# Optimization experiments

Measured on AMD Instinct MI355X. Metric: run time of the kernel, lower is better.

Reference implementation:

```python
import jax, jax.numpy as jnp
import numpy as np

WS = 8
NH = 6

def _ln(x, g, b, eps=1e-5):
    m = x.mean(-1, keepdims=True)
    v = jnp.var(x, axis=-1, keepdims=True)
    return (x - m) / jnp.sqrt(v + eps) * g + b

def _dwconv(x_nchw, k):
    # depthwise 3x3, stride 1, padding 1 (SAME); k: (C,1,3,3)
    return jax.lax.conv_general_dilated(
        x_nchw, k, (1, 1), 'SAME',
        dimension_numbers=('NCHW', 'OIHW', 'NCHW'),
        feature_group_count=x_nchw.shape[1])

def setup_inputs() -> dict:
    key = jax.random.key(0)
    ks = jax.random.split(key, 12)
    B, H, W, C = 2, 256, 256, 180
    hd_ffn = 360
    s = 0.02
    return {
        'x': jax.random.normal(ks[0], (B, H * W, C), jnp.float32),
        'w_qkv': jax.random.normal(ks[1], (3 * C, C), jnp.float32) * s,
        'b_rel': jax.random.normal(ks[2], (NH, WS * WS, WS * WS), jnp.float32) * s,
        'w_proj': jax.random.normal(ks[3], (C, C), jnp.float32) * s,
        'b_proj': jnp.zeros((C,), jnp.float32),
        'conv_dw': jax.random.normal(ks[4], (C, 1, 3, 3), jnp.float32) * 0.1,
        'cg_w1': jax.random.normal(ks[5], (C // 8, C), jnp.float32) * s,
        'cg_w2': jax.random.normal(ks[6], (C, C // 8), jnp.float32) * s,
        'ffn_w1': jax.random.normal(ks[7], (hd_ffn, C), jnp.float32) * s,
        'ffn_dw': jax.random.normal(ks[8], (hd_ffn, 1, 3, 3), jnp.float32) * 0.1,
        'ffn_w2': jax.random.normal(ks[9], (C, hd_ffn), jnp.float32) * s,
        'n1_g': jnp.ones((C,), jnp.float32),
        'n1_b': jnp.zeros((C,), jnp.float32),
        'n2_g': jnp.ones((C,), jnp.float32),
        'n2_b': jnp.zeros((C,), jnp.float32),
        'H': H,
        'W': W,
    }

def reference(x, w_qkv, b_rel, w_proj, b_proj, conv_dw, cg_w1, cg_w2,
              ffn_w1, ffn_dw, ffn_w2, n1_g, n1_b, n2_g, n2_b, H, W):
    B, L, C = x.shape
    hd = C // NH
    scale = hd ** -0.5
    n1 = _ln(x, n1_g, n1_b)
    # --- spatial window attention branch ---
    xw = n1.reshape(B, H // WS, WS, W // WS, WS, C)
    xw = xw.transpose(0, 1, 3, 2, 4, 5).reshape(-1, WS * WS, C)  # (nw, 64, C)
    qkv = (xw @ w_qkv.T).reshape(-1, WS * WS, 3, NH, hd).transpose(2, 0, 3, 1, 4)
    q, k, v = qkv[0], qkv[1], qkv[2]  # (nw, nh, 64, hd)
    attn = jax.nn.softmax((q * scale) @ jnp.swapaxes(k, -2, -1) + b_rel, axis=-1)
    out = (attn @ v).transpose(0, 2, 1, 3).reshape(-1, WS * WS, C)
    out = out @ w_proj.T + b_proj
    attn_feat = out.reshape(B, H // WS, W // WS, WS, WS, C)
    attn_feat = attn_feat.transpose(0, 1, 3, 2, 4, 5).reshape(B, L, C)
    # --- conv branch: depthwise 3x3 + GELU ---
    nchw = n1.transpose(0, 2, 1).reshape(B, C, H, W)
    conv_feat = jax.nn.gelu(_dwconv(nchw, conv_dw), approximate=False)
    conv_feat = conv_feat.reshape(B, C, L).transpose(0, 2, 1)
    # --- AIM: channel gate on conv_feat modulates attn_feat ---
    pooled = conv_feat.mean(axis=1)  # (B, C) == AdaptiveAvgPool2d(1)
    cm = jax.nn.sigmoid(jax.nn.gelu(pooled @ cg_w1.T, approximate=False) @ cg_w2.T)
    x = x + (attn_feat * cm[:, None, :] + conv_feat)
    # --- FFN with depthwise spatial mixing ---
    n2 = _ln(x, n2_g, n2_b)
    h = jax.nn.gelu(n2 @ ffn_w1.T, approximate=False)  # (B, L, hd_ffn)
    hdim = h.shape[-1]
    h_s = _dwconv(h.transpose(0, 2, 1).reshape(B, hdim, H, W), ffn_dw)
    h_s = h_s.reshape(B, hdim, L).transpose(0, 2, 1)
    return x + h_s @ ffn_w2.T
```

## Files before the change

kernel.cpp:

```cpp
#include <hip/hip_runtime.h>
#include <hip/hip_bf16.h>
#include <math.h>

#define BATCH 2
#define IMG 256
#define LTOK 65536
#define CH 180
#define BL (BATCH * LTOK)
#define HDF 360

using frag_ab = __attribute__((ext_vector_type(8))) short;
using frag_cd = __attribute__((ext_vector_type(4))) float;

__device__ __forceinline__ float b2f(unsigned short u) {
    union { unsigned int i; float f; } v; v.i = ((unsigned int)u) << 16; return v.f;
}
__device__ __forceinline__ float blo(unsigned int u) {
    union { unsigned int i; float f; } v; v.i = u << 16; return v.f;
}
__device__ __forceinline__ float bhi(unsigned int u) {
    union { unsigned int i; float f; } v; v.i = u & 0xffff0000u; return v.f;
}
__device__ __forceinline__ unsigned short f2b(float f) {
    union { float f; unsigned int i; } v; v.f = f;
    unsigned int x = v.i;
    unsigned int r = (x + 0x7fffu + ((x >> 16) & 1u)) >> 16;
    return (unsigned short)r;
}
__device__ __forceinline__ float gelu_f(float x) {
    return 0.5f * x * (1.0f + erff(x * 0.70710678118654752f));
}

template <int PERM>
__device__ __forceinline__ int perm_row(int row) {
    if (PERM == 1) {
        int b = row >> 16, l = row & 65535;
        int y = l >> 8, x = l & 255;
        return (b << 16) + ((((y >> 3) << 5) + (x >> 3)) << 6) + ((y & 7) << 3) + (x & 7);
    } else if (PERM == 2) {
        int b = row >> 16, wv = row & 65535;
        int wid = wv >> 6, t = wv & 63;
        int wy = wid >> 5, wx = wid & 31;
        return (b << 16) + ((((wy << 3) + (t >> 3))) << 8) + (wx << 3) + (t & 7);
    }
    return row;
}

__global__ __launch_bounds__(256) void convw_kernel(
    const float* __restrict__ a, const float* __restrict__ b,
    const float* __restrict__ c, const float* __restrict__ d,
    const float* __restrict__ cdw, const float* __restrict__ fdw,
    const float* __restrict__ brel,
    unsigned short* __restrict__ wbf, float* __restrict__ wT1, float* __restrict__ wT2,
    unsigned short* __restrict__ br3)
{
    int g = blockIdx.x * 256 + threadIdx.x;
    if (g < 259200) {
        float v;
        if      (g < 97200)  v = a[g];
        else if (g < 129600) v = b[g - 97200];
        else if (g < 194400) v = c[g - 129600];
        else                 v = d[g - 194400];
        wbf[g] = f2b(v);
    } else if (g < 265680) {
        int i = g - 259200;
        int tap = i / 180, ch = i % 180;
        wT1[i] = cdw[ch * 9 + tap];
    } else if (g < 278640) {
        int i = g - 265680;
        int tap = i / 360, ch = i % 360;
        wT2[i] = fdw[ch * 9 + tap];
    } else if (g < 303216) {
        int i = g - 278640;
        int h = i >> 12;
        int rem = i & 4095;
        int lane = rem >> 6;
        int j = rem & 63;
        int mt = j >> 4, nt = (j >> 2) & 3, r = j & 3;
        int row = mt * 16 + (lane >> 4) * 4 + r;
        int col = nt * 16 + (lane & 15);
        br3[i] = f2b(brel[h * 4096 + row * 64 + col]);
    }
}

__device__ __forceinline__ void ld4(const float* p, float v[4]) {
    float4 t = *(const float4*)p; v[0]=t.x; v[1]=t.y; v[2]=t.z; v[3]=t.w;
}
__device__ __forceinline__ void ld4(const unsigned short* p, float v[4]) {
    ushort4 t = *(const ushort4*)p; v[0]=b2f(t.x); v[1]=b2f(t.y); v[2]=b2f(t.z); v[3]=b2f(t.w);
}

template <typename TIN>
__global__ __launch_bounds__(256) void ln_kernel(
    const TIN* __restrict__ x, const float* __restrict__ g,
    const float* __restrict__ bta, unsigned short* __restrict__ out)
{
    int wave = threadIdx.x >> 6, lane = threadIdx.x & 63;
    int tok = blockIdx.x * 4 + wave;
    const bool act = lane < 45;
    float v[4] = {0.f, 0.f, 0.f, 0.f};
    const TIN* row = x + (size_t)tok * CH;
    if (act) ld4(row + lane * 4, v);
    float s  = v[0] + v[1] + v[2] + v[3];
    float sq = v[0]*v[0] + v[1]*v[1] + v[2]*v[2] + v[3]*v[3];
    #pragma unroll
    for (int off = 32; off > 0; off >>= 1) {
        s  += __shfl_xor(s, off);
        sq += __shfl_xor(sq, off);
    }
    float mean = s * (1.f / CH);
    float var  = sq * (1.f / CH) - mean * mean;
    float rstd = rsqrtf(var + 1e-5f);
    if (act) {
        float4 gg = *(const float4*)&g[lane * 4];
        float4 bb = *(const float4*)&bta[lane * 4];
        unsigned int o0 = (unsigned int)f2b((v[0]-mean)*rstd*gg.x + bb.x)
                        | ((unsigned int)f2b((v[1]-mean)*rstd*gg.y + bb.y) << 16);
        unsigned int o1 = (unsigned int)f2b((v[2]-mean)*rstd*gg.z + bb.z)
                        | ((unsigned int)f2b((v[3]-mean)*rstd*gg.w + bb.w) << 16);
        *(uint2*)(out + (size_t)tok * CH + lane * 4) = make_uint2(o0, o1);
    }
}

__device__ __forceinline__ void stv(float* p, float v) { *p = v; }
__device__ __forceinline__ void stv(unsigned short* p, float v) { *p = f2b(v); }

__device__ __forceinline__ frag_ab ldg_frag(const unsigned short* p) {
    union { frag_ab f; uint2 u[2]; } t;
    t.u[0] = *(const uint2*)p;
    t.u[1] = *(const uint2*)(p + 4);
    return t.f;
}
__device__ __forceinline__ frag_ab ldg_frag_tail(const unsigned short* p, int kcol0, int K) {
    union { frag_ab f; unsigned short s[8]; } t;
    #pragma unroll
    for (int j = 0; j < 8; ++j)
        t.s[j] = (kcol0 + j < K) ? p[j] : (unsigned short)0;
    return t.f;
}

template <int KT, int ACT, bool HAS_BIAS, bool HAS_RES, int PERM, typename TOUT>
__global__ __launch_bounds__(256) void gemm_kernel(
    const unsigned short* __restrict__ X, int ldx,
    const unsigned short* __restrict__ Wt,
    const float* __restrict__ bias,
    const unsigned short* __restrict__ res, int ldr,
    TOUT* __restrict__ Y, int ldy,
    int N)
{
    constexpr int NCH  = KT / 32;
    constexpr bool TAIL = (KT % 32) != 0;
    constexpr int NFR  = NCH + (TAIL ? 1 : 0);

    const int tid = threadIdx.x;
    const int wave = tid >> 6;
    const int lane = tid & 63;
    const int l16 = lane & 15;
    const int q = lane >> 4;
    const int m0 = blockIdx.x * 128;
    const int ktail0 = NCH * 32 + q * 8;

    frag_ab areg[2][NFR];
    {
        const unsigned short* aptr0 = X + (size_t)(m0 + wave * 32 + l16) * ldx + q * 8;
        const unsigned short* aptr1 = aptr0 + (size_t)16 * ldx;
        #pragma unroll
        for (int kc = 0; kc < NCH; ++kc) {
            areg[0][kc] = ldg_frag(aptr0 + kc * 32);
            areg[1][kc] = ldg_frag(aptr1 + kc * 32);
        }
        if (TAIL) {
            areg[0][NFR - 1] = ldg_frag_tail(aptr0 + NCH * 32, ktail0, KT);
            areg[1][NFR - 1] = ldg_frag_tail(aptr1 + NCH * 32, ktail0, KT);
        }
    }

    for (int n0 = 0; n0 < N; n0 += 64) {
        frag_cd acc[2][4];
        #pragma unroll
        for (int mb = 0; mb < 2; ++mb)
            #pragma unroll
            for (int nb = 0; nb < 4; ++nb)
                acc[mb][nb] = (frag_cd){0.f, 0.f, 0.f, 0.f};

        const unsigned short* bptr[4];
        #pragma unroll
        for (int nb = 0; nb < 4; ++nb)
            bptr[nb] = Wt + (size_t)(n0 + nb * 16 + l16) * KT + q * 8;

        #pragma unroll
        for (int kc = 0; kc < NCH; ++kc) {
            #pragma unroll
            for (int nb = 0; nb < 4; ++nb) {
                frag_ab b = ldg_frag(bptr[nb] + kc * 32);
                acc[0][nb] = __builtin_amdgcn_mfma_f32_16x16x32_bf16(areg[0][kc], b, acc[0][nb], 0, 0, 0);
                acc[1][nb] = __builtin_amdgcn_mfma_f32_16x16x32_bf16(areg[1][kc], b, acc[1][nb], 0, 0, 0);
            }
        }
        if (TAIL) {
            #pragma unroll
            for (int nb = 0; nb < 4; ++nb) {
                frag_ab b = ldg_frag_tail(bptr[nb] + NCH * 32, ktail0, KT);
                acc[0][nb] = __builtin_amdgcn_mfma_f32_16x16x32_bf16(areg[0][NFR - 1], b, acc[0][nb], 0, 0, 0);
                acc[1][nb] = __builtin_amdgcn_mfma_f32_16x16x32_bf16(areg[1][NFR - 1], b, acc[1][nb], 0, 0, 0);
            }
        }

        #pragma unroll
        for (int nb = 0; nb < 4; ++nb) {
            const int col = n0 + nb * 16 + l16;
            if (col < N) {
                float bv = 0.f;
                if (HAS_BIAS) bv = bias[col];
                #pragma unroll
                for (int mb = 0; mb < 2; ++mb) {
                    #pragma unroll
                    for (int r = 0; r < 4; ++r) {
                        int row = m0 + wave * 32 + mb * 16 + q * 4 + r;
                        int orow = perm_row<PERM>(row);
                        float v = acc[mb][nb][r] + bv;
                        if (ACT == 1) v = gelu_f(v);
                        if (HAS_RES) v += b2f(res[(size_t)orow * ldr + col]);
                        stv(&Y[(size_t)orow * ldy + col], v);
                    }
                }
            }
        }
    }
}

__global__ __launch_bounds__(64) void attn_kernel(
    const unsigned short* __restrict__ qkvw,
    const unsigned short* __restrict__ br3,
    unsigned short* __restrict__ attn_out)
{
    __shared__ unsigned short Pl[64][72];
    __shared__ unsigned short VT[32][72];
    const int blk = blockIdx.x;
    const int h = blk % 6;
    const int w = blk / 6;
    const int lane = threadIdx.x;
    const int l16 = lane & 15;
    const int g4 = lane >> 4;
    const float scale = 0.18257418583505536f;

    const unsigned short* base = qkvw + (size_t)w * (64 * 540) + h * 30;

    frag_ab qf[4], kf[4];
    #pragma unroll
    for (int t = 0; t < 4; ++t) {
        const unsigned short* pq = base + (size_t)(t * 16 + l16) * 540 + g4 * 8;
        union { frag_ab f; uint2 u[2]; } tq, tk;
        tq.u[0] = *(const uint2*)pq;        tq.u[1] = *(const uint2*)(pq + 4);
        tk.u[0] = *(const uint2*)(pq + 180); tk.u[1] = *(const uint2*)(pq + 184);
        if (g4 == 3) { tk.f[6] = 0; tk.f[7] = 0; }
        qf[t] = tq.f; kf[t] = tk.f;
    }

    unsigned int brw[32];
    {
        const unsigned short* bp = br3 + ((size_t)h << 12) + lane * 64;
        #pragma unroll
        for (int c2 = 0; c2 < 8; ++c2)
            *(uint4*)&brw[c2 * 4] = *(const uint4*)(bp + c2 * 8);
    }

    frag_cd s[4][4];
    #pragma unroll
    for (int mt = 0; mt < 4; ++mt)
        #pragma unroll
        for (int nt = 0; nt < 4; ++nt)
            s[mt][nt] = (frag_cd){0.f, 0.f, 0.f, 0.f};
    #pragma unroll
    for (int mt = 0; mt < 4; ++mt)
        #pragma unroll
        for (int nt = 0; nt < 4; ++nt)
            s[mt][nt] = __builtin_amdgcn_mfma_f32_16x16x32_bf16(qf[mt], kf[nt], s[mt][nt], 0, 0, 0);

    {
        const unsigned short* pv = base + (size_t)lane * 540 + 360;
        #pragma unroll
        for (int d2 = 0; d2 < 15; ++d2) {
            unsigned int u = *(const unsigned int*)(pv + 2 * d2);
            VT[2 * d2][lane]     = (unsigned short)(u & 0xffffu);
            VT[2 * d2 + 1][lane] = (unsigned short)(u >> 16);
        }
        VT[30][lane] = 0; VT[31][lane] = 0;
    }

    float inv[4][4];
    #pragma unroll
    for (int mt = 0; mt < 4; ++mt) {
        #pragma unroll
        for (int r = 0; r < 4; ++r) {
            float a0 = s[mt][0][r] * scale + (((0 * 4 + r) & 1) ? bhi(brw[(mt * 16 + 0 + r) >> 1]) : blo(brw[(mt * 16 + 0 + r) >> 1]));
            float a1 = s[mt][1][r] * scale + (((1 * 4 + r) & 1) ? bhi(brw[(mt * 16 + 4 + r) >> 1]) : blo(brw[(mt * 16 + 4 + r) >> 1]));
            float a2 = s[mt][2][r] * scale + (((2 * 4 + r) & 1) ? bhi(brw[(mt * 16 + 8 + r) >> 1]) : blo(brw[(mt * 16 + 8 + r) >> 1]));
            float a3 = s[mt][3][r] * scale + (((3 * 4 + r) & 1) ? bhi(brw[(mt * 16 + 12 + r) >> 1]) : blo(brw[(mt * 16 + 12 + r) >> 1]));
            float m = fmaxf(fmaxf(a0, a1), fmaxf(a2, a3));
            m = fmaxf(m, __shfl_xor(m, 1));
            m = fmaxf(m, __shfl_xor(m, 2));
            m = fmaxf(m, __shfl_xor(m, 4));
            m = fmaxf(m, __shfl_xor(m, 8));
            float e0 = __expf(a0 - m), e1 = __expf(a1 - m);
            float e2 = __expf(a2 - m), e3 = __expf(a3 - m);
            float sum = e0 + e1 + e2 + e3;
            sum += __shfl_xor(sum, 1);
            sum += __shfl_xor(sum, 2);
            sum += __shfl_xor(sum, 4);
            sum += __shfl_xor(sum, 8);
            inv[mt][r] = 1.f / sum;
            int row = mt * 16 + g4 * 4 + r;
            Pl[row][l16]      = f2b(e0);
            Pl[row][16 + l16] = f2b(e1);
            Pl[row][32 + l16] = f2b(e2);
            Pl[row][48 + l16] = f2b(e3);
        }
    }
    __syncthreads();

    frag_ab pf[4][2];
    #pragma unroll
    for (int mt = 0; mt < 4; ++mt)
        #pragma unroll
        for (int kt = 0; kt < 2; ++kt)
            pf[mt][kt] = *(const frag_ab*)&Pl[mt * 16 + l16][kt * 32 + g4 * 8];
    frag_ab vf[2][2];
    #pragma unroll
    for (int nt = 0; nt < 2; ++nt)
        #pragma unroll
        for (int kt = 0; kt < 2; ++kt)
            vf[nt][kt] = *(const frag_ab*)&VT[nt * 16 + l16][kt * 32 + g4 * 8];

    frag_cd o[4][2];
    #pragma unroll
    for (int mt = 0; mt < 4; ++mt)
        #pragma unroll
        for (int nt = 0; nt < 2; ++nt)
            o[mt][nt] = (frag_cd){0.f, 0.f, 0.f, 0.f};
    #pragma unroll
    for (int mt = 0; mt < 4; ++mt)
        #pragma unroll
        for (int nt = 0; nt < 2; ++nt)
            #pragma unroll
            for (int kt = 0; kt < 2; ++kt)
                o[mt][nt] = __builtin_amdgcn_mfma_f32_16x16x32_bf16(pf[mt][kt], vf[nt][kt], o[mt][nt], 0, 0, 0);

    unsigned short* ob = attn_out + (size_t)w * (64 * CH) + h * 30;
    #pragma unroll
    for (int mt = 0; mt < 4; ++mt) {
        #pragma unroll
        for (int r = 0; r < 4; ++r) {
            int row = mt * 16 + g4 * 4 + r;
            float iv = inv[mt][r];
            unsigned short* op = ob + (size_t)row * CH;
            op[l16] = f2b(o[mt][0][r] * iv);
            if (l16 < 14) op[16 + l16] = f2b(o[mt][1][r] * iv);
        }
    }
}

template <int C, bool DO_GELU>
__global__ __launch_bounds__(256) void dwconv_kernel(
    const unsigned short* __restrict__ in, const float* __restrict__ wT,
    unsigned short* __restrict__ out)
{
    constexpr int NG = (C + 7) / 8;
    constexpr int TY = 8;
    int gid = blockIdx.x * 256 + threadIdx.x;
    int cg = gid % NG;
    int t  = gid / NG;
    int x  = t % IMG;
    int t2 = t / IMG;
    int yb = t2 & 31;
    int bi = t2 >> 5;
    if (bi >= BATCH) return;
    const int c0 = cg * 8;
    const int y0 = yb * TY;

    float w9[9][8];
    #pragma unroll
    for (int tp = 0; tp < 9; ++tp) {
        float4 wa = *(const float4*)&wT[tp * C + c0];
        float4 wb = *(const float4*)&wT[tp * C + c0 + 4];
        w9[tp][0]=wa.x; w9[tp][1]=wa.y; w9[tp][2]=wa.z; w9[tp][3]=wa.w;
        w9[tp][4]=wb.x; w9[tp][5]=wb.y; w9[tp][6]=wb.z; w9[tp][7]=wb.w;
    }

    unsigned int rr[3][3][4];

    auto load_row = [&](int y, unsigned int dst[3][4]) {
        if ((unsigned)y >= (unsigned)IMG) {
            #pragma unroll
            for (int cc = 0; cc < 3; ++cc)
                #pragma unroll
                for (int k = 0; k < 4; ++k) dst[cc][k] = 0u;
            return;
        }
        size_t base = ((size_t)((bi << 16) + (y << 8) + x)) * C + c0;
        #pragma unroll
        for (int cc = 0; cc < 3; ++cc) {
            int xx = x + cc - 1;
            if ((unsigned)xx >= (unsigned)IMG) {
                dst[cc][0] = dst[cc][1] = dst[cc][2] = dst[cc][3] = 0u;
                continue;
            }
            const unsigned short* p = in + base + (ptrdiff_t)(cc - 1) * C;
            uint2 u0 = *(const uint2*)p;
            uint2 u1 = *(const uint2*)(p + 4);
            dst[cc][0] = u0.x; dst[cc][1] = u0.y; dst[cc][2] = u1.x; dst[cc][3] = u1.y;
        }
    };

    load_row(y0 - 1, rr[0]);
    load_row(y0,     rr[1]);

    #pragma unroll
    for (int dy = 0; dy < TY; ++dy) {
        load_row(y0 + dy + 1, rr[(dy + 2) % 3]);
        float acc[8];
        #pragma unroll
        for (int j = 0; j < 8; ++j) acc[j] = 0.f;
        #pragma unroll
        for (int ky = 0; ky < 3; ++ky) {
            unsigned int (*row)[4] = rr[(dy + ky) % 3];
            #pragma unroll
            for (int kx = 0; kx < 3; ++kx) {
                const float* wp = w9[ky * 3 + kx];
                const unsigned int* u = row[kx];
                acc[0] += blo(u[0]) * wp[0];
                acc[1] += bhi(u[0]) * wp[1];
                acc[2] += blo(u[1]) * wp[2];
                acc[3] += bhi(u[1]) * wp[3];
                acc[4] += blo(u[2]) * wp[4];
                acc[5] += bhi(u[2]) * wp[5];
                acc[6] += blo(u[3]) * wp[6];
                acc[7] += bhi(u[3]) * wp[7];
            }
        }
        if (DO_GELU) {
            #pragma unroll
            for (int j = 0; j < 8; ++j) acc[j] = gelu_f(acc[j]);
        }
        size_t ob = ((size_t)((bi << 16) + ((y0 + dy) << 8) + x)) * C + c0;
        unsigned int o0 = (unsigned int)f2b(acc[0]) | ((unsigned int)f2b(acc[1]) << 16);
        unsigned int o1 = (unsigned int)f2b(acc[2]) | ((unsigned int)f2b(acc[3]) << 16);
        *(uint2*)(out + ob) = make_uint2(o0, o1);
        if (c0 + 8 <= C) {
            unsigned int o2 = (unsigned int)f2b(acc[4]) | ((unsigned int)f2b(acc[5]) << 16);
            unsigned int o3 = (unsigned int)f2b(acc[6]) | ((unsigned int)f2b(acc[7]) << 16);
            *(uint2*)(out + ob + 4) = make_uint2(o2, o3);
        }
    }
}

__global__ __launch_bounds__(64) void pool_kernel(
    const unsigned short* __restrict__ cf, float* __restrict__ pooled)
{
    int t = threadIdx.x;
    if (t >= 45) return;
    int b = blockIdx.x >> 7;
    int chunk = blockIdx.x & 127;
    const unsigned short* base = cf + (size_t)(b * LTOK + chunk * 512) * CH + t * 4;
    float s0 = 0.f, s1 = 0.f, s2 = 0.f, s3 = 0.f;
    for (int i = 0; i < 512; ++i) {
        ushort4 v = *(const ushort4*)(base + (size_t)i * CH);
        s0 += b2f(v.x); s1 += b2f(v.y); s2 += b2f(v.z); s3 += b2f(v.w);
    }
    atomicAdd(&pooled[b * CH + t * 4 + 0], s0);
    atomicAdd(&pooled[b * CH + t * 4 + 1], s1);
    atomicAdd(&pooled[b * CH + t * 4 + 2], s2);
    atomicAdd(&pooled[b * CH + t * 4 + 3], s3);
}

__global__ __launch_bounds__(256) void cm_kernel(
    const float* __restrict__ pooled, const float* __restrict__ w1,
    const float* __restrict__ w2, float* __restrict__ cm)
{
    __shared__ float p[BATCH][CH];
    __shared__ float g1[BATCH][22];
    int t = threadIdx.x;
    for (int idx = t; idx < BATCH * CH; idx += 256)
        p[idx / CH][idx % CH] = pooled[idx] * (1.f / (float)LTOK);
    __syncthreads();
    if (t < BATCH * 22) {
        int b = t / 22, u = t % 22;
        float s = 0.f;
        for (int c = 0; c < CH; ++c) s += p[b][c] * w1[u * CH + c];
        g1[b][u] = gelu_f(s);
    }
    __syncthreads();
    for (int idx = t; idx < BATCH * CH; idx += 256) {
        int b = idx / CH, c = idx % CH;
        float s = 0.f;
        for (int u = 0; u < 22; ++u) s += g1[b][u] * w2[c * 22 + u];
        cm[idx] = 1.f / (1.f + __expf(-s));
    }
}

__global__ __launch_bounds__(256) void resid_kernel(
    const float* __restrict__ x, const unsigned short* __restrict__ attn_feat,
    const unsigned short* __restrict__ conv_feat, const float* __restrict__ cm,
    unsigned short* __restrict__ x_mid)
{
    int gid = blockIdx.x * 256 + threadIdx.x;
    int c4 = gid % 45;
    int b = gid / (LTOK * 45);
    float4 xv = ((const float4*)x)[gid];
    ushort4 a = ((const ushort4*)attn_feat)[gid];
    ushort4 c = ((const ushort4*)conv_feat)[gid];
    float4 m = *(const float4*)&cm[b * CH + c4 * 4];
    unsigned int o0 = (unsigned int)f2b(xv.x + b2f(a.x) * m.x + b2f(c.x))
                    | ((unsigned int)f2b(xv.y + b2f(a.y) * m.y + b2f(c.y)) << 16);
    unsigned int o1 = (unsigned int)f2b(xv.z + b2f(a.z) * m.z + b2f(c.z))
                    | ((unsigned int)f2b(xv.w + b2f(a.w) * m.w + b2f(c.w)) << 16);
    ((uint2*)x_mid)[gid] = make_uint2(o0, o1);
}

extern "C" void kernel_launch(void* const* d_in, const int* in_sizes, int n_in,
                              void* d_out, int out_size, void* d_ws, size_t ws_size,
                              hipStream_t stream)
{
    const float* x       = (const float*)d_in[0];
    const float* w_qkv   = (const float*)d_in[1];
    const float* b_rel   = (const float*)d_in[2];
    const float* w_proj  = (const float*)d_in[3];
    const float* b_proj  = (const float*)d_in[4];
    const float* conv_dw = (const float*)d_in[5];
    const float* cg_w1   = (const float*)d_in[6];
    const float* cg_w2   = (const float*)d_in[7];
    const float* ffn_w1  = (const float*)d_in[8];
    const float* ffn_dw  = (const float*)d_in[9];
    const float* ffn_w2  = (const float*)d_in[10];
    const float* n1_g    = (const float*)d_in[11];
    const float* n1_b    = (const float*)d_in[12];
    const float* n2_g    = (const float*)d_in[13];
    const float* n2_b    = (const float*)d_in[14];

    char* ws = (char*)d_ws;
    unsigned short* n1        = (unsigned short*)(ws);
    unsigned short* qkvw      = (unsigned short*)(ws + 47185920);
    unsigned short* conv_feat = (unsigned short*)(ws + 188743680);
    unsigned short* attn_out  = (unsigned short*)(ws);
    unsigned short* attn_feat = (unsigned short*)(ws + 47185920);
    unsigned short* x_mid     = (unsigned short*)(ws + 94371840);
    unsigned short* n2        = (unsigned short*)(ws + 141557760);
    unsigned short* h         = (unsigned short*)(ws);
    unsigned short* h_s       = (unsigned short*)(ws + 141557760);
    float*          pooled    = (float*)(ws + 235929600);
    float*          cmv       = (float*)(ws + 235931040);
    unsigned short* wbf       = (unsigned short*)(ws + 235932480);
    float*          wT1       = (float*)(ws + 236450880);
    float*          wT2       = (float*)(ws + 236476800);
    unsigned short* br3       = (unsigned short*)(ws + 236528640);
    unsigned short* wqkv_b  = wbf;
    unsigned short* wproj_b = wbf + 97200;
    unsigned short* wffn1_b = wbf + 129600;
    unsigned short* wffn2_b = wbf + 194400;
    float* out = (float*)d_out;

    hipMemsetAsync(pooled, 0, 2880, stream);

    convw_kernel<<<1185, 256, 0, stream>>>(w_qkv, w_proj, ffn_w1, ffn_w2,
                                           conv_dw, ffn_dw, b_rel, wbf, wT1, wT2, br3);
    ln_kernel<float><<<BL / 4, 256, 0, stream>>>(x, n1_g, n1_b, n1);
    gemm_kernel<180, 0, false, false, 1, unsigned short><<<BL / 128, 256, 0, stream>>>(
        n1, CH, wqkv_b, nullptr, nullptr, 0, qkvw, 540, 540);
    dwconv_kernel<CH, true><<<1472, 256, 0, stream>>>(n1, wT1, conv_feat);
    pool_kernel<<<BATCH * 128, 64, 0, stream>>>(conv_feat, pooled);
    cm_kernel<<<1, 256, 0, stream>>>(pooled, cg_w1, cg_w2, cmv);
    attn_kernel<<<2048 * 6, 64, 0, stream>>>(qkvw, br3, attn_out);
    gemm_kernel<180, 0, true, false, 2, unsigned short><<<BL / 128, 256, 0, stream>>>(
        attn_out, CH, wproj_b, b_proj, nullptr, 0, attn_feat, CH, CH);
    resid_kernel<<<(BL * CH / 4) / 256, 256, 0, stream>>>(x, attn_feat, conv_feat, cmv, x_mid);
    ln_kernel<unsigned short><<<BL / 4, 256, 0, stream>>>(x_mid, n2_g, n2_b, n2);
    gemm_kernel<180, 1, false, false, 0, unsigned short><<<BL / 128, 256, 0, stream>>>(
        n2, CH, wffn1_b, nullptr, nullptr, 0, h, HDF, HDF);
    dwconv_kernel<HDF, false><<<2880, 256, 0, stream>>>(h, wT2, h_s);
    gemm_kernel<360, 0, false, true, 0, float><<<BL / 128, 256, 0, stream>>>(
        h_s, HDF, wffn2_b, nullptr, x_mid, CH, out, CH, CH);
}
```

Baseline: 951.2 us.

## Fuse QKV projection into window attention and fuse residual with LayerNorm2

Replaces the separate QKV GEMM and per-head attention kernel with one kernel per 8x8 window. It loads the window's n1 rows into registers, computes Q/K/V per head with MFMA into LDS, then runs softmax attention, so the large bf16 qkv intermediate is never written to or read from global memory. The residual-add kernel and the second LayerNorm are also merged into one pass, saving a reread of x_mid. The cost is that each block re-reads the whole QKV weight matrix from global/L2 and serialises the six heads with three barriers per head. The workspace buffers are rearranged to fit.

```diff
diff --git a/kernel.cpp b/kernel.cpp
--- a/kernel.cpp
+++ b/kernel.cpp
@@ -52,7 +52,7 @@
     const float* __restrict__ cdw, const float* __restrict__ fdw,
     const float* __restrict__ brel,
     unsigned short* __restrict__ wbf, float* __restrict__ wT1, float* __restrict__ wT2,
-    unsigned short* __restrict__ br3)
+    unsigned short* __restrict__ br4)
 {
     int g = blockIdx.x * 256 + threadIdx.x;
     if (g < 259200) {
@@ -74,20 +74,18 @@
         int i = g - 278640;
         int h = i >> 12;
         int rem = i & 4095;
-        int lane = rem >> 6;
-        int j = rem & 63;
-        int mt = j >> 4, nt = (j >> 2) & 3, r = j & 3;
-        int row = mt * 16 + (lane >> 4) * 4 + r;
-        int col = nt * 16 + (lane & 15);
-        br3[i] = f2b(brel[h * 4096 + row * 64 + col]);
+        int tid = rem >> 4;
+        int j = rem & 15;
+        int nt = j >> 2, r = j & 3;
+        int w = tid >> 6, q = (tid >> 4) & 3, l16 = tid & 15;
+        int row = w * 16 + q * 4 + r;
+        int col = nt * 16 + l16;
+        br4[i] = f2b(brel[h * 4096 + row * 64 + col]);
     }
 }
 
 __device__ __forceinline__ void ld4(const float* p, float v[4]) {
     float4 t = *(const float4*)p; v[0]=t.x; v[1]=t.y; v[2]=t.z; v[3]=t.w;
-}
-__device__ __forceinline__ void ld4(const unsigned short* p, float v[4]) {
-    ushort4 t = *(const ushort4*)p; v[0]=b2f(t.x); v[1]=b2f(t.y); v[2]=b2f(t.z); v[3]=b2f(t.w);
 }
 
 template <typename TIN>
@@ -229,74 +227,100 @@
     }
 }
 
-__global__ __launch_bounds__(64) void attn_kernel(
-    const unsigned short* __restrict__ qkvw,
-    const unsigned short* __restrict__ br3,
+__global__ __launch_bounds__(256) void qkvattn_kernel(
+    const unsigned short* __restrict__ n1,
+    const unsigned short* __restrict__ wqkv,
+    const unsigned short* __restrict__ br4,
     unsigned short* __restrict__ attn_out)
 {
-    __shared__ unsigned short Pl[64][72];
+    __shared__ unsigned short Klds[64][40];
     __shared__ unsigned short VT[32][72];
+    __shared__ unsigned short Qlds[4][16][40];
+    __shared__ unsigned short Pl[4][16][72];
+
     const int blk = blockIdx.x;
-    const int h = blk % 6;
-    const int w = blk / 6;
-    const int lane = threadIdx.x;
+    const int b = blk >> 10;
+    const int wid = blk & 1023;
+    const int wy = wid >> 5, wx = wid & 31;
+    const int tid = threadIdx.x;
+    const int wave = tid >> 6;
+    const int lane = tid & 63;
     const int l16 = lane & 15;
-    const int g4 = lane >> 4;
+    const int q = lane >> 4;
     const float scale = 0.18257418583505536f;
 
-    const unsigned short* base = qkvw + (size_t)w * (64 * 540) + h * 30;
-
-    frag_ab qf[4], kf[4];
-    #pragma unroll
-    for (int t = 0; t < 4; ++t) {
-        const unsigned short* pq = base + (size_t)(t * 16 + l16) * 540 + g4 * 8;
-        union { frag_ab f; uint2 u[2]; } tq, tk;
-        tq.u[0] = *(const uint2*)pq;        tq.u[1] = *(const uint2*)(pq + 4);
-        tk.u[0] = *(const uint2*)(pq + 180); tk.u[1] = *(const uint2*)(pq + 184);
-        if (g4 == 3) { tk.f[6] = 0; tk.f[7] = 0; }
-        qf[t] = tq.f; kf[t] = tk.f;
-    }
-
-    unsigned int brw[32];
+    frag_ab areg[6];
     {
-        const unsigned short* bp = br3 + ((size_t)h << 12) + lane * 64;
-        #pragma unroll
-        for (int c2 = 0; c2 < 8; ++c2)
-            *(uint4*)&brw[c2 * 4] = *(const uint4*)(bp + c2 * 8);
-    }
-
-    frag_cd s[4][4];
-    #pragma unroll
-    for (int mt = 0; mt < 4; ++mt)
-        #pragma unroll
-        for (int nt = 0; nt < 4; ++nt)
-            s[mt][nt] = (frag_cd){0.f, 0.f, 0.f, 0.f};
-    #pragma unroll
-    for (int mt = 0; mt < 4; ++mt)
-        #pragma unroll
-        for (int nt = 0; nt < 4; ++nt)
-            s[mt][nt] = __builtin_amdgcn_mfma_f32_16x16x32_bf16(qf[mt], kf[nt], s[mt][nt], 0, 0, 0);
-
-    {
-        const unsigned short* pv = base + (size_t)lane * 540 + 360;
-        #pragma unroll
-        for (int d2 = 0; d2 < 15; ++d2) {
-            unsigned int u = *(const unsigned int*)(pv + 2 * d2);
-            VT[2 * d2][lane]     = (unsigned short)(u & 0xffffu);
-            VT[2 * d2 + 1][lane] = (unsigned short)(u >> 16);
-        }
-        VT[30][lane] = 0; VT[31][lane] = 0;
-    }
-
-    float inv[4][4];
-    #pragma unroll
-    for (int mt = 0; mt < 4; ++mt) {
+        int t = wave * 16 + l16;
+        size_t grow = ((size_t)b << 16) + (size_t)((wy * 8 + (t >> 3)) << 8) + wx * 8 + (t & 7);
+        const unsigned short* ap = n1 + grow * CH + q * 8;
+        #pragma unroll
+        for (int kc = 0; kc < 5; ++kc) areg[kc] = ldg_frag(ap + kc * 32);
+        areg[5] = ldg_frag_tail(ap + 160, 160 + q * 8, CH);
+    }
+
+    for (int h = 0; h < 6; ++h) {
+        unsigned int brw[8];
+        {
+            const unsigned short* bp = br4 + ((size_t)h << 12) + tid * 16;
+            *(uint4*)&brw[0] = *(const uint4*)bp;
+            *(uint4*)&brw[4] = *(const uint4*)(bp + 8);
+        }
+
+        #pragma unroll
+        for (int s = 0; s < 3; ++s) {
+            const unsigned short* wp0 = wqkv + (size_t)(s * 180 + h * 30 + l16) * CH + q * 8;
+            const unsigned short* wp1 = wp0 + (size_t)16 * CH;
+            frag_cd ac0 = (frag_cd){0.f, 0.f, 0.f, 0.f};
+            frag_cd ac1 = (frag_cd){0.f, 0.f, 0.f, 0.f};
+            #pragma unroll
+            for (int kc = 0; kc < 5; ++kc) {
+                frag_ab b0 = ldg_frag(wp0 + kc * 32);
+                frag_ab b1 = ldg_frag(wp1 + kc * 32);
+                ac0 = __builtin_amdgcn_mfma_f32_16x16x32_bf16(areg[kc], b0, ac0, 0, 0, 0);
+                ac1 = __builtin_amdgcn_mfma_f32_16x16x32_bf16(areg[kc], b1, ac1, 0, 0, 0);
+            }
+            {
+                frag_ab b0 = ldg_frag_tail(wp0 + 160, 160 + q * 8, CH);
+                frag_ab b1 = ldg_frag_tail(wp1 + 160, 160 + q * 8, CH);
+                ac0 = __builtin_amdgcn_mfma_f32_16x16x32_bf16(areg[5], b0, ac0, 0, 0, 0);
+                ac1 = __builtin_amdgcn_mfma_f32_16x16x32_bf16(areg[5], b1, ac1, 0, 0, 0);
+            }
+            #pragma unroll
+            for (int r = 0; r < 4; ++r) {
+                unsigned short v0 = f2b(ac0[r]);
+                unsigned short v1 = (l16 >= 14) ? (unsigned short)0 : f2b(ac1[r]);
+                int rr = wave * 16 + q * 4 + r;
+                if (s == 0) {
+                    Qlds[wave][q * 4 + r][l16]      = v0;
+                    Qlds[wave][q * 4 + r][16 + l16] = v1;
+                } else if (s == 1) {
+                    Klds[rr][l16]      = v0;
+                    Klds[rr][16 + l16] = v1;
+                } else {
+                    VT[l16][rr]      = v0;
+                    VT[16 + l16][rr] = v1;
+                }
+            }
+        }
+        __syncthreads();
+
+        frag_ab qf = *(const frag_ab*)&Qlds[wave][l16][q * 8];
+        frag_cd s4[4];
+        #pragma unroll
+        for (int nt = 0; nt < 4; ++nt) {
+            frag_ab kf = *(const frag_ab*)&Klds[nt * 16 + l16][q * 8];
+            s4[nt] = __builtin_amdgcn_mfma_f32_16x16x32_bf16(
+                qf, kf, (frag_cd){0.f, 0.f, 0.f, 0.f}, 0, 0, 0);
+        }
+
+        float inv[4];
         #pragma unroll
         for (int r = 0; r < 4; ++r) {
-            float a0 = s[mt][0][r] * scale + (((0 * 4 + r) & 1) ? bhi(brw[(mt * 16 + 0 + r) >> 1]) : blo(brw[(mt * 16 + 0 + r) >> 1]));
-            float a1 = s[mt][1][r] * scale + (((1 * 4 + r) & 1) ? bhi(brw[(mt * 16 + 4 + r) >> 1]) : blo(brw[(mt * 16 + 4 + r) >> 1]));
-            float a2 = s[mt][2][r] * scale + (((2 * 4 + r) & 1) ? bhi(brw[(mt * 16 + 8 + r) >> 1]) : blo(brw[(mt * 16 + 8 + r) >> 1]));
-            float a3 = s[mt][3][r] * scale + (((3 * 4 + r) & 1) ? bhi(brw[(mt * 16 + 12 + r) >> 1]) : blo(brw[(mt * 16 + 12 + r) >> 1]));
+            float a0 = s4[0][r] * scale + ((r & 1) ? bhi(brw[0 + (r >> 1)]) : blo(brw[0 + (r >> 1)]));
+            float a1 = s4[1][r] * scale + ((r & 1) ? bhi(brw[2 + (r >> 1)]) : blo(brw[2 + (r >> 1)]));
+            float a2 = s4[2][r] * scale + ((r & 1) ? bhi(brw[4 + (r >> 1)]) : blo(brw[4 + (r >> 1)]));
+            float a3 = s4[3][r] * scale + ((r & 1) ? bhi(brw[6 + (r >> 1)]) : blo(brw[6 + (r >> 1)]));
             float m = fmaxf(fmaxf(a0, a1), fmaxf(a2, a3));
             m = fmaxf(m, __shfl_xor(m, 1));
             m = fmaxf(m, __shfl_xor(m, 2));
@@ -309,54 +333,37 @@
             sum += __shfl_xor(sum, 2);
             sum += __shfl_xor(sum, 4);
             sum += __shfl_xor(sum, 8);
-            inv[mt][r] = 1.f / sum;
-            int row = mt * 16 + g4 * 4 + r;
-            Pl[row][l16]      = f2b(e0);
-            Pl[row][16 + l16] = f2b(e1);
-            Pl[row][32 + l16] = f2b(e2);
-            Pl[row][48 + l16] = f2b(e3);
-        }
-    }
-    __syncthreads();
-
-    frag_ab pf[4][2];
-    #pragma unroll
-    for (int mt = 0; mt < 4; ++mt)
-        #pragma unroll
-        for (int kt = 0; kt < 2; ++kt)
-            pf[mt][kt] = *(const frag_ab*)&Pl[mt * 16 + l16][kt * 32 + g4 * 8];
-    frag_ab vf[2][2];
-    #pragma unroll
-    for (int nt = 0; nt < 2; ++nt)
-        #pragma unroll
-        for (int kt = 0; kt < 2; ++kt)
-            vf[nt][kt] = *(const frag_ab*)&VT[nt * 16 + l16][kt * 32 + g4 * 8];
-
-    frag_cd o[4][2];
-    #pragma unroll
-    for (int mt = 0; mt < 4; ++mt)
-        #pragma unroll
-        for (int nt = 0; nt < 2; ++nt)
-            o[mt][nt] = (frag_cd){0.f, 0.f, 0.f, 0.f};
-    #pragma unroll
-    for (int mt = 0; mt < 4; ++mt)
-        #pragma unroll
-        for (int nt = 0; nt < 2; ++nt)
-            #pragma unroll
-            for (int kt = 0; kt < 2; ++kt)
-                o[mt][nt] = __builtin_amdgcn_mfma_f32_16x16x32_bf16(pf[mt][kt], vf[nt][kt], o[mt][nt], 0, 0, 0);
-
-    unsigned short* ob = attn_out + (size_t)w * (64 * CH) + h * 30;
-    #pragma unroll
-    for (int mt = 0; mt < 4; ++mt) {
+            inv[r] = 1.f / sum;
+            int pr = q * 4 + r;
+            Pl[wave][pr][l16]      = f2b(e0);
+            Pl[wave][pr][16 + l16] = f2b(e1);
+            Pl[wave][pr][32 + l16] = f2b(e2);
+            Pl[wave][pr][48 + l16] = f2b(e3);
+        }
+        __syncthreads();
+
+        frag_ab pf0 = *(const frag_ab*)&Pl[wave][l16][q * 8];
+        frag_ab pf1 = *(const frag_ab*)&Pl[wave][l16][32 + q * 8];
+        frag_ab v00 = *(const frag_ab*)&VT[l16][q * 8];
+        frag_ab v01 = *(const frag_ab*)&VT[l16][32 + q * 8];
+        frag_ab v10 = *(const frag_ab*)&VT[16 + l16][q * 8];
+        frag_ab v11 = *(const frag_ab*)&VT[16 + l16][32 + q * 8];
+        frag_cd o0 = (frag_cd){0.f, 0.f, 0.f, 0.f};
+        frag_cd o1 = (frag_cd){0.f, 0.f, 0.f, 0.f};
+        o0 = __builtin_amdgcn_mfma_f32_16x16x32_bf16(pf0, v00, o0, 0, 0, 0);
+        o0 = __builtin_amdgcn_mfma_f32_16x16x32_bf16(pf1, v01, o0, 0, 0, 0);
+        o1 = __builtin_amdgcn_mfma_f32_16x16x32_bf16(pf0, v10, o1, 0, 0, 0);
+        o1 = __builtin_amdgcn_mfma_f32_16x16x32_bf16(pf1, v11, o1, 0, 0, 0);
+
+        unsigned short* ob = attn_out + ((size_t)blk * 64 + wave * 16) * CH + h * 30;
         #pragma unroll
         for (int r = 0; r < 4; ++r) {
-            int row = mt * 16 + g4 * 4 + r;
-            float iv = inv[mt][r];
-            unsigned short* op = ob + (size_t)row * CH;
-            op[l16] = f2b(o[mt][0][r] * iv);
-            if (l16 < 14) op[16 + l16] = f2b(o[mt][1][r] * iv);
-        }
+            float iv = inv[r];
+            unsigned short* op = ob + (size_t)(q * 4 + r) * CH;
+            op[l16] = f2b(o0[r] * iv);
+            if (l16 < 14) op[16 + l16] = f2b(o1[r] * iv);
+        }
+        __syncthreads();
     }
 }
 
@@ -498,23 +505,51 @@
     }
 }
 
-__global__ __launch_bounds__(256) void resid_kernel(
+__global__ __launch_bounds__(256) void resid_ln2_kernel(
     const float* __restrict__ x, const unsigned short* __restrict__ attn_feat,
     const unsigned short* __restrict__ conv_feat, const float* __restrict__ cm,
-    unsigned short* __restrict__ x_mid)
-{
-    int gid = blockIdx.x * 256 + threadIdx.x;
-    int c4 = gid % 45;
-    int b = gid / (LTOK * 45);
-    float4 xv = ((const float4*)x)[gid];
-    ushort4 a = ((const ushort4*)attn_feat)[gid];
-    ushort4 c = ((const ushort4*)conv_feat)[gid];
-    float4 m = *(const float4*)&cm[b * CH + c4 * 4];
-    unsigned int o0 = (unsigned int)f2b(xv.x + b2f(a.x) * m.x + b2f(c.x))
-                    | ((unsigned int)f2b(xv.y + b2f(a.y) * m.y + b2f(c.y)) << 16);
-    unsigned int o1 = (unsigned int)f2b(xv.z + b2f(a.z) * m.z + b2f(c.z))
-                    | ((unsigned int)f2b(xv.w + b2f(a.w) * m.w + b2f(c.w)) << 16);
-    ((uint2*)x_mid)[gid] = make_uint2(o0, o1);
+    const float* __restrict__ g, const float* __restrict__ bta,
+    unsigned short* __restrict__ x_mid, unsigned short* __restrict__ n2)
+{
+    int wave = threadIdx.x >> 6, lane = threadIdx.x & 63;
+    int tok = blockIdx.x * 4 + wave;
+    const bool act = lane < 45;
+    float v[4] = {0.f, 0.f, 0.f, 0.f};
+    if (act) {
+        size_t base = (size_t)tok * CH + lane * 4;
+        float4 xv = *(const float4*)&x[base];
+        ushort4 a = *(const ushort4*)&attn_feat[base];
+        ushort4 c = *(const ushort4*)&conv_feat[base];
+        int b = tok >> 16;
+        float4 m = *(const float4*)&cm[b * CH + lane * 4];
+        unsigned short u0 = f2b(xv.x + b2f(a.x) * m.x + b2f(c.x));
+        unsigned short u1 = f2b(xv.y + b2f(a.y) * m.y + b2f(c.y));
+        unsigned short u2 = f2b(xv.z + b2f(a.z) * m.z + b2f(c.z));
+        unsigned short u3 = f2b(xv.w + b2f(a.w) * m.w + b2f(c.w));
+        *(uint2*)(x_mid + base) = make_uint2(
+            (unsigned int)u0 | ((unsigned int)u1 << 16),
+            (unsigned int)u2 | ((unsigned int)u3 << 16));
+        v[0] = b2f(u0); v[1] = b2f(u1); v[2] = b2f(u2); v[3] = b2f(u3);
+    }
+    float s  = v[0] + v[1] + v[2] + v[3];
+    float sq = v[0]*v[0] + v[1]*v[1] + v[2]*v[2] + v[3]*v[3];
+    #pragma unroll
+    for (int off = 32; off > 0; off >>= 1) {
+        s  += __shfl_xor(s, off);
+        sq += __shfl_xor(sq, off);
+    }
+    float mean = s * (1.f / CH);
+    float var  = sq * (1.f / CH) - mean * mean;
+    float rstd = rsqrtf(var + 1e-5f);
+    if (act) {
+        float4 gg = *(const float4*)&g[lane * 4];
+        float4 bb = *(const float4*)&bta[lane * 4];
+        unsigned int o0 = (unsigned int)f2b((v[0]-mean)*rstd*gg.x + bb.x)
+                        | ((unsigned int)f2b((v[1]-mean)*rstd*gg.y + bb.y) << 16);
+        unsigned int o1 = (unsigned int)f2b((v[2]-mean)*rstd*gg.z + bb.z)
+                        | ((unsigned int)f2b((v[3]-mean)*rstd*gg.w + bb.w) << 16);
+        *(uint2*)(n2 + (size_t)tok * CH + lane * 4) = make_uint2(o0, o1);
+    }
 }
 
 extern "C" void kernel_launch(void* const* d_in, const int* in_sizes, int n_in,
@@ -539,20 +574,19 @@
 
     char* ws = (char*)d_ws;
     unsigned short* n1        = (unsigned short*)(ws);
-    unsigned short* qkvw      = (unsigned short*)(ws + 47185920);
+    unsigned short* x_mid     = (unsigned short*)(ws);
+    unsigned short* attn_out  = (unsigned short*)(ws + 47185920);
+    unsigned short* attn_feat = (unsigned short*)(ws + 94371840);
+    unsigned short* h         = (unsigned short*)(ws + 47185920);
+    unsigned short* n2        = (unsigned short*)(ws + 141557760);
+    unsigned short* h_s       = (unsigned short*)(ws + 141557760);
     unsigned short* conv_feat = (unsigned short*)(ws + 188743680);
-    unsigned short* attn_out  = (unsigned short*)(ws);
-    unsigned short* attn_feat = (unsigned short*)(ws + 47185920);
-    unsigned short* x_mid     = (unsigned short*)(ws + 94371840);
-    unsigned short* n2        = (unsigned short*)(ws + 141557760);
-    unsigned short* h         = (unsigned short*)(ws);
-    unsigned short* h_s       = (unsigned short*)(ws + 141557760);
     float*          pooled    = (float*)(ws + 235929600);
     float*          cmv       = (float*)(ws + 235931040);
     unsigned short* wbf       = (unsigned short*)(ws + 235932480);
     float*          wT1       = (float*)(ws + 236450880);
     float*          wT2       = (float*)(ws + 236476800);
-    unsigned short* br3       = (unsigned short*)(ws + 236528640);
+    unsigned short* br4       = (unsigned short*)(ws + 236528640);
     unsigned short* wqkv_b  = wbf;
     unsigned short* wproj_b = wbf + 97200;
     unsigned short* wffn1_b = wbf + 129600;
@@ -562,18 +596,16 @@
     hipMemsetAsync(pooled, 0, 2880, stream);
 
     convw_kernel<<<1185, 256, 0, stream>>>(w_qkv, w_proj, ffn_w1, ffn_w2,
-                                           conv_dw, ffn_dw, b_rel, wbf, wT1, wT2, br3);
+                                           conv_dw, ffn_dw, b_rel, wbf, wT1, wT2, br4);
     ln_kernel<float><<<BL / 4, 256, 0, stream>>>(x, n1_g, n1_b, n1);
-    gemm_kernel<180, 0, false, false, 1, unsigned short><<<BL / 128, 256, 0, stream>>>(
-        n1, CH, wqkv_b, nullptr, nullptr, 0, qkvw, 540, 540);
+    qkvattn_kernel<<<2048, 256, 0, stream>>>(n1, wqkv_b, br4, attn_out);
     dwconv_kernel<CH, true><<<1472, 256, 0, stream>>>(n1, wT1, conv_feat);
     pool_kernel<<<BATCH * 128, 64, 0, stream>>>(conv_feat, pooled);
     cm_kernel<<<1, 256, 0, stream>>>(pooled, cg_w1, cg_w2, cmv);
-    attn_kernel<<<2048 * 6, 64, 0, stream>>>(qkvw, br3, attn_out);
     gemm_kernel<180, 0, true, false, 2, unsigned short><<<BL / 128, 256, 0, stream>>>(
         attn_out, CH, wproj_b, b_proj, nullptr, 0, attn_feat, CH, CH);
-    resid_kernel<<<(BL * CH / 4) / 256, 256, 0, stream>>>(x, attn_feat, conv_feat, cmv, x_mid);
-    ln_kernel<unsigned short><<<BL / 4, 256, 0, stream>>>(x_mid, n2_g, n2_b, n2);
+    resid_ln2_kernel<<<BL / 4, 256, 0, stream>>>(x, attn_feat, conv_feat, cmv,
+                                                 n2_g, n2_b, x_mid, n2);
     gemm_kernel<180, 1, false, false, 0, unsigned short><<<BL / 128, 256, 0, stream>>>(
         n2, CH, wffn1_b, nullptr, nullptr, 0, h, HDF, HDF);
     dwconv_kernel<HDF, false><<<2880, 256, 0, stream>>>(h, wT2, h_s);
```

New measurement: 915.5 us. 3.7% less time.
